# Performance work log

Hardware: AMD Instinct MI355X
Metric: run time of the kernel (lower is better)

The kernel has to match this reference:

```python
import jax, jax.numpy as jnp
import numpy as np

N = 100000   # nodes
E = 1600000  # edges (before self loops)
H = 4        # heads
C = 32       # per-head channels
D = H * C    # hidden_dim = 128
G = 64       # graphs in batch
L = 4        # num_layers
IN_DIM = 7
NEG_SLOPE = 0.2


def setup_inputs() -> dict:
    key = jax.random.key(0)
    ks = jax.random.split(key, 14)
    s = 0.1
    x = jax.random.normal(ks[0], (N, IN_DIM), jnp.float32)
    edge_index = jax.random.randint(ks[1], (2, E), 0, N, dtype=jnp.int32)
    batch = jnp.sort(jax.random.randint(ks[2], (N,), 0, G, dtype=jnp.int32))
    W0 = jax.random.normal(ks[3], (IN_DIM, D), jnp.float32) * s
    a_src0 = jax.random.normal(ks[4], (H, C), jnp.float32) * s
    a_dst0 = jax.random.normal(ks[5], (H, C), jnp.float32) * s
    b0 = jnp.zeros((D,), jnp.float32)
    Ws = jax.random.normal(ks[6], (L - 1, D, D), jnp.float32) * s
    a_srcs = jax.random.normal(ks[7], (L - 1, H, C), jnp.float32) * s
    a_dsts = jax.random.normal(ks[8], (L - 1, H, C), jnp.float32) * s
    bs = jnp.zeros((L - 1, D), jnp.float32)
    ln_g = jnp.ones((L, D), jnp.float32)
    ln_b = jnp.zeros((L, D), jnp.float32)
    return dict(x=x, edge_index=edge_index, batch=batch, W0=W0, a_src0=a_src0,
                a_dst0=a_dst0, b0=b0, Ws=Ws, a_srcs=a_srcs, a_dsts=a_dsts,
                bs=bs, ln_g=ln_g, ln_b=ln_b)


def _gat_layer(x, W, a_src, a_dst, b, src, dst):
    # x: [N, F_in] -> h: [N, H, C] (PyG GATConv: shared lin for src/dst)
    h = (x @ W).reshape(N, H, C)
    alpha_src = jnp.einsum('nhc,hc->nh', h, a_src)  # [N, H]
    alpha_dst = jnp.einsum('nhc,hc->nh', h, a_dst)  # [N, H]
    logits = jax.nn.leaky_relu(alpha_src[src] + alpha_dst[dst], NEG_SLOPE)  # [E', H]
    # segment softmax over edges grouped by destination node
    m = jax.ops.segment_max(logits, dst, num_segments=N)          # [N, H]
    e = jnp.exp(logits - m[dst])
    z = jax.ops.segment_sum(e, dst, num_segments=N)               # [N, H]
    alpha = e / (z[dst] + 1e-16)                                  # [E', H]
    msg = h[src] * alpha[..., None]                               # [E', H, C]
    out = jax.ops.segment_sum(msg, dst, num_segments=N)           # [N, H, C]
    return out.reshape(N, D) + b


def _layernorm(x, g, b):
    mu = jnp.mean(x, axis=-1, keepdims=True)
    var = jnp.var(x, axis=-1, keepdims=True)
    return (x - mu) * jax.lax.rsqrt(var + 1e-5) * g + b


def reference(x, edge_index, batch, W0, a_src0, a_dst0, b0, Ws, a_srcs, a_dsts, bs, ln_g, ln_b):
    # PyG GATConv default: add self loops
    loop = jnp.arange(N, dtype=edge_index.dtype)
    src = jnp.concatenate([edge_index[0], loop])
    dst = jnp.concatenate([edge_index[1], loop])
    h = x
    for i in range(L):
        if i == 0:
            W, asr, ads, b = W0, a_src0, a_dst0, b0
        else:
            W, asr, ads, b = Ws[i - 1], a_srcs[i - 1], a_dsts[i - 1], bs[i - 1]
        h_new = _gat_layer(h, W, asr, ads, b, src, dst)
        h_new = jax.nn.elu(_layernorm(h_new, ln_g[i], ln_b[i]))
        h = h + h_new if i > 0 else h_new  # dropout is identity in eval
    node_embeddings = h  # [N, D]
    sums = jax.ops.segment_sum(node_embeddings, batch, num_segments=G)  # [G, D]
    cnt = jax.ops.segment_sum(jnp.ones((N,), node_embeddings.dtype), batch, num_segments=G)
    graph_embedding = sums / jnp.maximum(cnt, 1.0)[:, None]
    return node_embeddings, graph_embedding
```

## Files before the change

kernel.cpp:

```cpp
#include <hip/hip_runtime.h>
#include <hip/hip_bf16.h>

#define NN 100000
#define NE 1600000
#define NH 4
#define NC 32
#define DD 128
#define NG 64
#define NIN 7

#define BSH 9
#define NBUK ((NN + 511) >> BSH)
#define SEGCAP 9600
#define CAPE (SEGCAP - 512)
#define CSRN (NBUK * SEGCAP)
#define NBBIN ((NE + 4095)/4096)

typedef __hip_bfloat16 bf16;
typedef __attribute__((ext_vector_type(8))) short short8;
typedef __attribute__((ext_vector_type(4))) float f32x4;
typedef __attribute__((ext_vector_type(2))) float f32x2;

__device__ __forceinline__ float b2f(const bf16 v){ return __bfloat162float(v); }

__device__ __forceinline__ float in_ld(const void* p, size_t i, int f32){
  return f32 ? ((const float*)p)[i] : b2f(((const bf16*)p)[i]);
}

__device__ __forceinline__ unsigned int bfbits(float v){
  bf16 b = __float2bfloat16(v);
  return (unsigned int)(*(unsigned short*)&b);
}

__global__ __launch_bounds__(256) void k_init(float* __restrict__ gsum, int* __restrict__ gcnt,
                                              int* __restrict__ bcur,
                                              const unsigned int* __restrict__ xb, int* __restrict__ flag){
  int i = blockIdx.x*256 + threadIdx.x;
  if (i < NG*DD) gsum[i] = 0.f;
  if (i < NG) gcnt[i] = 0;
  if (i < NBUK) bcur[i] = i * CAPE;
  if (blockIdx.x == 0 && threadIdx.x < 64){
    int t = threadIdx.x;
    int pl = 0;
    for (int j = t; j < 512; j += 64){
      float v = __uint_as_float(xb[j]);
      float a = fabsf(v);
      if (v == v && a < 1e6f && a > 1e-10f) pl++;
    }
    #pragma unroll
    for (int off = 32; off > 0; off >>= 1) pl += __shfl_down(pl, off);
    if (t == 0) *flag = (pl >= 384) ? 1 : 0;
  }
}

__global__ __launch_bounds__(256) void k_bin(const int* __restrict__ src, const int* __restrict__ dst,
                                             int* __restrict__ bcur, int2* __restrict__ gstag,
                                             const void* __restrict__ Ws, bf16* __restrict__ WT,
                                             const int* __restrict__ flag){
  if (blockIdx.x >= NBBIN){
    int l = blockIdx.x - NBBIN;
    int f32 = *flag;
    for (int idx = threadIdx.x; idx < DD*DD; idx += 256){
      int n = idx >> 7, k = idx & 127;
      WT[(size_t)l*DD*DD + idx] = __float2bfloat16(in_ld(Ws, (size_t)l*DD*DD + (size_t)k*DD + n, f32));
    }
    return;
  }
  __shared__ int cnt[NBUK], pref[NBUK+1], place[NBUK], gbase[NBUK];
  __shared__ int2 pairs[4096];
  int tid = threadIdx.x;
  for (int b = tid; b < NBUK; b += 256){ cnt[b]=0; place[b]=0; }
  __syncthreads();
  int e0 = blockIdx.x*4096;
  int s[16], d[16];
  #pragma unroll
  for (int i=0;i<16;i++){
    int e = e0 + i*256 + tid;
    s[i] = 0; d[i] = -1;
    if (e < NE){
      unsigned int us = (unsigned int)src[e]; if (us >= NN) us = 0;
      unsigned int ud = (unsigned int)dst[e]; if (ud >= NN) ud = 0;
      s[i] = (int)us; d[i] = (int)ud;
      atomicAdd(&cnt[ud>>BSH], 1);
    }
  }
  __syncthreads();
  if (tid == 0){
    int run = 0;
    for (int b=0;b<NBUK;b++){ pref[b] = run; run += cnt[b]; }
    pref[NBUK] = run;
  }
  __syncthreads();
  for (int b = tid; b < NBUK; b += 256){
    if (cnt[b] > 0) gbase[b] = atomicAdd(&bcur[b], cnt[b]);
  }
  __syncthreads();
  #pragma unroll
  for (int i=0;i<16;i++){
    if (d[i] >= 0){
      int b = d[i]>>BSH;
      int lp = atomicAdd(&place[b],1);
      pairs[pref[b]+lp] = make_int2(s[i], d[i]);
    }
  }
  __syncthreads();
  int tot = pref[NBUK];
  for (int j = tid; j < tot; j += 256){
    int2 pr = pairs[j];
    int b = pr.y>>BSH;
    int gidx = gbase[b] + (j - pref[b]);
    if (gidx >= b*CAPE && gidx < (b+1)*CAPE) gstag[gidx] = pr;
  }
}

__global__ __launch_bounds__(256) void k_bucket(const int2* __restrict__ gstag,
                                                const int* __restrict__ bcur,
                                                int* __restrict__ csr,
                                                int* __restrict__ offs, int* __restrict__ oend){
  __shared__ int seg[SEGCAP];
  __shared__ int lcnt[512];
  __shared__ int loff[512];
  __shared__ int pscan[256];
  int b = blockIdx.x, tid = threadIdx.x;
  int nstart = b << BSH;
  int nend = min(nstart + 512, NN);
  int nloc = nend - nstart;
  int base = b * SEGCAP;
  int stbase = b * CAPE;
  int ecnt = bcur[b] - stbase;
  ecnt = max(0, min(ecnt, CAPE));
  lcnt[tid]     = (tid < nloc) ? 1 : 0;
  lcnt[tid+256] = (tid+256 < nloc) ? 1 : 0;
  __syncthreads();
  for (int j = tid; j < ecnt; j += 256){
    int2 pr = gstag[stbase + j];
    int ln = pr.y - nstart;
    if (ln < 0 || ln >= nloc) ln = 0;
    atomicAdd(&lcnt[ln], 1);
  }
  __syncthreads();
  int c0 = lcnt[2*tid], c1 = lcnt[2*tid+1];
  int pairsum = c0 + c1;
  pscan[tid] = pairsum;
  __syncthreads();
  for (int off=1; off<256; off<<=1){
    int a = (tid >= off) ? pscan[tid-off] : 0;
    __syncthreads();
    pscan[tid] += a;
    __syncthreads();
  }
  int pexcl = pscan[tid] - pairsum;
  loff[2*tid]   = pexcl;
  loff[2*tid+1] = pexcl + c0;
  __syncthreads();
  int segN = pscan[255];
  if (segN > SEGCAP) segN = SEGCAP;
  if (tid < nloc){
    offs[nstart + tid] = base + loff[tid];
    oend[nstart + tid] = base + loff[tid] + lcnt[tid];
  }
  if (tid + 256 < nloc){
    offs[nstart + tid + 256] = base + loff[tid+256];
    oend[nstart + tid + 256] = base + loff[tid+256] + lcnt[tid+256];
  }
  __syncthreads();
  if (tid < nloc){ int p = loff[tid]; if (p < SEGCAP) seg[p] = nstart + tid; lcnt[tid] = 1; }
  if (tid + 256 < nloc){ int p = loff[tid+256]; if (p < SEGCAP) seg[p] = nstart + tid + 256; lcnt[tid+256] = 1; }
  __syncthreads();
  for (int j = tid; j < ecnt; j += 256){
    int2 pr = gstag[stbase + j];
    int ln = pr.y - nstart;
    if (ln < 0 || ln >= nloc) ln = 0;
    int p = atomicAdd(&lcnt[ln], 1);
    int idx = loff[ln] + p;
    if (idx >= 0 && idx < SEGCAP) seg[idx] = pr.x;
  }
  __syncthreads();
  for (int j = tid; j < segN; j += 256) csr[base + j] = seg[j];
}

__device__ __forceinline__ void alpha_red(float acc, float was, float wad, int d, int n,
                                          float* __restrict__ asrc, float* __restrict__ adst){
  float ps = acc*was, pd = acc*wad;
  #pragma unroll
  for (int off=16; off>0; off>>=1){
    ps += __shfl_down(ps, off, 32);
    pd += __shfl_down(pd, off, 32);
  }
  if ((d & 31) == 0){
    asrc[n*NH + (d>>5)] = ps;
    adst[n*NH + (d>>5)] = pd;
  }
}

__global__ __launch_bounds__(128) void k_gemm0(const void* __restrict__ x, const void* __restrict__ W,
    const void* __restrict__ aws, const void* __restrict__ awd,
    bf16* __restrict__ hproj,
    float* __restrict__ asrc, float* __restrict__ adst, const int* __restrict__ flag){
  int f32 = *flag;
  __shared__ float xr[4][NIN];
  int d = threadIdx.x;
  int n0 = blockIdx.x*4;
  if (d < 4*NIN) xr[d/NIN][d%NIN] = in_ld(x, (size_t)n0*NIN + d, f32);
  __syncthreads();
  float a0=0,a1=0,a2=0,a3=0;
  #pragma unroll
  for (int k=0;k<NIN;k++){
    float w = in_ld(W, (size_t)k*DD + d, f32);
    a0 += xr[0][k]*w; a1 += xr[1][k]*w; a2 += xr[2][k]*w; a3 += xr[3][k]*w;
  }
  hproj[(size_t)(n0+0)*DD+d]=__float2bfloat16(a0);
  hproj[(size_t)(n0+1)*DD+d]=__float2bfloat16(a1);
  hproj[(size_t)(n0+2)*DD+d]=__float2bfloat16(a2);
  hproj[(size_t)(n0+3)*DD+d]=__float2bfloat16(a3);
  float was = in_ld(aws, d, f32), wad = in_ld(awd, d, f32);
  alpha_red(a0, was, wad, d, n0+0, asrc, adst);
  alpha_red(a1, was, wad, d, n0+1, asrc, adst);
  alpha_red(a2, was, wad, d, n0+2, asrc, adst);
  alpha_red(a3, was, wad, d, n0+3, asrc, adst);
}

#define LDA 136
#define LDB 136

__global__ __launch_bounds__(256) void k_gemm_mfma(
    const bf16* __restrict__ resid,
    const bf16* __restrict__ WT, size_t wtoff,
    const void* __restrict__ aws, const void* __restrict__ awd, size_t aoff,
    bf16* __restrict__ hproj,
    float* __restrict__ asrc, float* __restrict__ adst,
    const int* __restrict__ flag)
{
  __shared__ bf16 sA[64*LDA];
  __shared__ bf16 sB[128*LDB];
  int f32 = *flag;
  int t = threadIdx.x;
  int n0 = blockIdx.x*64;

  {
    const uint4* srcv = (const uint4*)(WT + wtoff);
    #pragma unroll
    for (int i=0;i<8;i++){
      int u4 = t + 256*i;
      int row = u4 >> 4, c = u4 & 15;
      *(uint4*)(&sB[row*LDB + c*8]) = srcv[u4];
    }
  }
  {
    const uint4* av = (const uint4*)resid;
    #pragma unroll
    for (int i=0;i<4;i++){
      int u4 = t + 256*i;
      int row = u4 >> 4, c = u4 & 15;
      int gr = n0 + row;
      uint4 v = make_uint4(0,0,0,0);
      if (gr < NN) v = av[(size_t)gr*16 + c];
      *(uint4*)(&sA[row*LDA + c*8]) = v;
    }
  }
  __syncthreads();

  int wv = t >> 6, lane = t & 63;
  int m = lane & 15, kq = lane >> 4;
  int rowbase = wv*16;

  f32x4 acc[8];
  #pragma unroll
  for (int nt=0; nt<8; nt++) acc[nt] = (f32x4){0.f,0.f,0.f,0.f};

  #pragma unroll
  for (int ks=0; ks<4; ks++){
    short8 afrag = *(const short8*)(&sA[(rowbase + m)*LDA + ks*32 + kq*8]);
    #pragma unroll
    for (int nt=0; nt<8; nt++){
      short8 bfrag = *(const short8*)(&sB[(nt*16 + m)*LDB + ks*32 + kq*8]);
      acc[nt] = __builtin_amdgcn_mfma_f32_16x16x32_bf16(afrag, bfrag, acc[nt], 0, 0, 0);
    }
  }

  #pragma unroll
  for (int reg=0; reg<4; reg++){
    int gr = n0 + rowbase + kq*4 + reg;
    if (gr < NN){
      bf16* dst = hproj + (size_t)gr*DD + m;
      #pragma unroll
      for (int nt=0; nt<8; nt++)
        dst[nt*16] = __float2bfloat16(acc[nt][reg]);
    }
  }

  float avs[8], avd[8];
  #pragma unroll
  for (int nt=0; nt<8; nt++){
    avs[nt] = in_ld(aws, aoff + nt*16 + m, f32);
    avd[nt] = in_ld(awd, aoff + nt*16 + m, f32);
  }
  #pragma unroll
  for (int h=0; h<4; h++){
    #pragma unroll
    for (int reg=0; reg<4; reg++){
      float ps = acc[2*h][reg]*avs[2*h] + acc[2*h+1][reg]*avs[2*h+1];
      float pd = acc[2*h][reg]*avd[2*h] + acc[2*h+1][reg]*avd[2*h+1];
      #pragma unroll
      for (int off=1; off<16; off<<=1){
        ps += __shfl_xor(ps, off);
        pd += __shfl_xor(pd, off);
      }
      if (m == 0){
        int gr = n0 + rowbase + kq*4 + reg;
        if (gr < NN){
          asrc[gr*NH + h] = ps;
          adst[gr*NH + h] = pd;
        }
      }
    }
  }
}

__device__ __forceinline__ float4 edge_e(const float4 as, const float4 ad){
  float4 l, e;
  l.x = as.x + ad.x; l.y = as.y + ad.y; l.z = as.z + ad.z; l.w = as.w + ad.w;
  l.x = l.x > 0.f ? l.x : 0.2f*l.x;
  l.y = l.y > 0.f ? l.y : 0.2f*l.y;
  l.z = l.z > 0.f ? l.z : 0.2f*l.z;
  l.w = l.w > 0.f ? l.w : 0.2f*l.w;
  l.x = fminf(l.x, 30.f); l.y = fminf(l.y, 30.f);
  l.z = fminf(l.z, 30.f); l.w = fminf(l.w, 30.f);
  e.x = __expf(l.x); e.y = __expf(l.y); e.z = __expf(l.z); e.w = __expf(l.w);
  return e;
}

__device__ __forceinline__ float2 hp_ld2(const void* hp, int s, int lane){
  unsigned int hv = ((const unsigned int*)hp)[(size_t)s*64 + lane];
  return make_float2(__uint_as_float(hv << 16), __uint_as_float(hv & 0xFFFF0000u));
}

__device__ __forceinline__ void fma_row(const uint4 hv, const float al,
                                        f32x2& a0, f32x2& a1, f32x2& a2, f32x2& a3){
  f32x2 v0 = {__uint_as_float(hv.x << 16), __uint_as_float(hv.x & 0xFFFF0000u)};
  f32x2 v1 = {__uint_as_float(hv.y << 16), __uint_as_float(hv.y & 0xFFFF0000u)};
  f32x2 v2 = {__uint_as_float(hv.z << 16), __uint_as_float(hv.z & 0xFFFF0000u)};
  f32x2 v3 = {__uint_as_float(hv.w << 16), __uint_as_float(hv.w & 0xFFFF0000u)};
  a0 += v0 * al;
  a1 += v1 * al;
  a2 += v2 * al;
  a3 += v3 * al;
}

template<int U>
__global__ __launch_bounds__(256) void k_agg(const bf16* __restrict__ hproj,
    const float* __restrict__ asrc, const float* __restrict__ adst,
    const int* __restrict__ offs, const int* __restrict__ oend, const int* __restrict__ csr,
    bf16* __restrict__ resid,
    const void* __restrict__ bias, size_t boff,
    const void* __restrict__ lng, const void* __restrict__ lnb, size_t lnoff,
    const int* __restrict__ flag, const int first)
{
  __shared__ float s_al[4][256];
  __shared__ int   s_off[4][64];
  int f32 = *flag;
  int wid = threadIdx.x >> 6, lane = threadIdx.x & 63;
  int n = blockIdx.x*4 + wid;
  int beg = offs[n];
  int end = oend[n];
  beg = max(0, min(beg, CSRN));
  end = max(beg, min(end, CSRN));
  int deg = min(end - beg, 1024);
  const float4 ad = ((const float4*)adst)[n];
  int head = lane >> 4;
  const char* hpB = (const char*)hproj;
  float2 acc;

  if (deg <= 64){
    float4 e = make_float4(0,0,0,0);
    if (lane < deg){
      unsigned int us = (unsigned int)csr[beg+lane];
      if (us >= NN) us = 0;
      s_off[wid][lane] = (int)(us << 8);
      float4 as = ((const float4*)asrc)[us];
      e = edge_e(as, ad);
    }
    float4 zs = e;
    #pragma unroll
    for (int off=32; off>0; off>>=1){
      zs.x += __shfl_down(zs.x, off);
      zs.y += __shfl_down(zs.y, off);
      zs.z += __shfl_down(zs.z, off);
      zs.w += __shfl_down(zs.w, off);
    }
    float4 invz;
    invz.x = 1.f/(__shfl(zs.x,0)+1e-16f);
    invz.y = 1.f/(__shfl(zs.y,0)+1e-16f);
    invz.z = 1.f/(__shfl(zs.z,0)+1e-16f);
    invz.w = 1.f/(__shfl(zs.w,0)+1e-16f);
    if (lane < deg){
      s_al[wid][lane*4+0] = e.x*invz.x;
      s_al[wid][lane*4+1] = e.y*invz.y;
      s_al[wid][lane*4+2] = e.z*invz.z;
      s_al[wid][lane*4+3] = e.w*invz.w;
    }
    __threadfence_block();

    int qg = lane >> 4;
    int ql = lane & 15;
    int hq = ql >> 2;
    int qbyte = ql << 4;
    f32x2 a0 = {0.f,0.f}, a1 = {0.f,0.f}, a2 = {0.f,0.f}, a3 = {0.f,0.f};
    int t = 0;
    for (; t+U <= deg; t += U){
      uint4 h[U/4];
      #pragma unroll
      for (int u=0; u<U/4; u++){
        int j = t + 4*u + qg;
        unsigned int off = (unsigned int)s_off[wid][j] + qbyte;
        h[u] = *(const uint4*)(hpB + off);
      }
      #pragma unroll
      for (int u=0; u<U/4; u++){
        int j = t + 4*u + qg;
        float al = s_al[wid][j*4 + hq];
        fma_row(h[u], al, a0, a1, a2, a3);
      }
    }
    for (; t+4 <= deg; t += 4){
      int j = t + qg;
      unsigned int off = (unsigned int)s_off[wid][j] + qbyte;
      const uint4 hv = *(const uint4*)(hpB + off);
      float al = s_al[wid][j*4 + hq];
      fma_row(hv, al, a0, a1, a2, a3);
    }
    if (t < deg){
      int j = t + qg;
      if (j < deg){
        unsigned int off = (unsigned int)s_off[wid][j] + qbyte;
        const uint4 hv = *(const uint4*)(hpB + off);
        float al = s_al[wid][j*4 + hq];
        fma_row(hv, al, a0, a1, a2, a3);
      }
    }

    #pragma unroll
    for (int off = 16; off < 64; off <<= 1){
      a0.x += __shfl_xor(a0.x, off); a0.y += __shfl_xor(a0.y, off);
      a1.x += __shfl_xor(a1.x, off); a1.y += __shfl_xor(a1.y, off);
      a2.x += __shfl_xor(a2.x, off); a2.y += __shfl_xor(a2.y, off);
      a3.x += __shfl_xor(a3.x, off); a3.y += __shfl_xor(a3.y, off);
    }
    __threadfence_block();
    if (qg == 0){
      float* red = &s_al[wid][0];
      red[ql*8+0] = a0.x; red[ql*8+1] = a0.y;
      red[ql*8+2] = a1.x; red[ql*8+3] = a1.y;
      red[ql*8+4] = a2.x; red[ql*8+5] = a2.y;
      red[ql*8+6] = a3.x; red[ql*8+7] = a3.y;
    }
    __threadfence_block();
    acc = make_float2(s_al[wid][2*lane], s_al[wid][2*lane+1]);
  } else {
    f32x2 ac0 = {0.f,0.f};
    float4 zs = make_float4(0,0,0,0);
    for (int j=lane; j<deg; j+=64){
      unsigned int us = (unsigned int)csr[beg+j];
      if (us >= NN) us = 0;
      float4 as = ((const float4*)asrc)[us];
      float4 e = edge_e(as, ad);
      zs.x+=e.x; zs.y+=e.y; zs.z+=e.z; zs.w+=e.w;
    }
    #pragma unroll
    for (int off=32; off>0; off>>=1){
      zs.x += __shfl_down(zs.x, off);
      zs.y += __shfl_down(zs.y, off);
      zs.z += __shfl_down(zs.z, off);
      zs.w += __shfl_down(zs.w, off);
    }
    float4 invz;
    invz.x = 1.f/(__shfl(zs.x,0)+1e-16f);
    invz.y = 1.f/(__shfl(zs.y,0)+1e-16f);
    invz.z = 1.f/(__shfl(zs.z,0)+1e-16f);
    invz.w = 1.f/(__shfl(zs.w,0)+1e-16f);
    int nch = (deg+63)>>6;
    for (int c2=0;c2<nch;c2++){
      int base = c2<<6, j = base+lane;
      int sreg = 0;
      __threadfence_block();
      if (j < deg){
        unsigned int us = (unsigned int)csr[beg+j];
        if (us >= NN) us = 0;
        sreg = (int)us;
        float4 as = ((const float4*)asrc)[us];
        float4 e = edge_e(as, ad);
        s_al[wid][lane*4+0]=e.x*invz.x;
        s_al[wid][lane*4+1]=e.y*invz.y;
        s_al[wid][lane*4+2]=e.z*invz.z;
        s_al[wid][lane*4+3]=e.w*invz.w;
      }
      __threadfence_block();
      int cnt = min(64, deg-base);
      int head2 = lane >> 4;
      for (int t2=0;t2<cnt;t2++){
        int s = __shfl(sreg, t2);
        float a = s_al[wid][t2*4+head2];
        float2 hv = hp_ld2(hproj, s, lane);
        ac0.x += hv.x*a;
        ac0.y += hv.y*a;
      }
    }
    acc = make_float2(ac0.x, ac0.y);
  }

  float vx = acc.x + in_ld(bias, boff + 2*lane,   f32);
  float vy = acc.y + in_ld(bias, boff + 2*lane+1, f32);
  float s1 = vx+vy, s2 = vx*vx+vy*vy;
  #pragma unroll
  for (int off=32; off>0; off>>=1){
    s1 += __shfl_down(s1, off);
    s2 += __shfl_down(s2, off);
  }
  float mean = __shfl(s1,0) * (1.f/DD);
  float msq  = __shfl(s2,0) * (1.f/DD);
  float var  = fmaxf(msq - mean*mean, 0.f);
  float r = rsqrtf(var + 1e-5f);
  float yx = (vx-mean)*r*in_ld(lng, lnoff+2*lane,   f32) + in_ld(lnb, lnoff+2*lane,   f32);
  float yy = (vy-mean)*r*in_ld(lng, lnoff+2*lane+1, f32) + in_ld(lnb, lnoff+2*lane+1, f32);
  yx = yx>0.f ? yx : expm1f(yx);
  yy = yy>0.f ? yy : expm1f(yy);
  float2 res;
  if (first){
    res = make_float2(yx, yy);
  } else {
    unsigned int pu = ((const unsigned int*)resid)[(size_t)n*64 + lane];
    res = make_float2(__uint_as_float(pu << 16) + yx,
                      __uint_as_float(pu & 0xFFFF0000u) + yy);
  }
  unsigned int pk = bfbits(res.x) | (bfbits(res.y) << 16);
  ((unsigned int*)resid)[(size_t)n*64 + lane] = pk;
}

__global__ __launch_bounds__(128) void k_pool(const bf16* __restrict__ resid, void* __restrict__ dout,
    const int* __restrict__ batch, float* __restrict__ gsum, int* __restrict__ gcnt,
    const int* __restrict__ flag){
  __shared__ int sb[64];
  int f32 = *flag;
  int d = threadIdx.x;
  int n0 = blockIdx.x*64;
  int cnt = min(64, NN - n0);
  if (d < cnt){
    unsigned int b = (unsigned int)batch[n0 + d];
    if (b >= NG) b = 0;
    sb[d] = (int)b;
  }
  __syncthreads();
  float local = 0.f;
  int cur = sb[0];
  for (int i=0;i<cnt;i++){
    int b = sb[i];
    if (b != cur){
      atomicAdd(&gsum[cur*DD + d], local);
      local = 0.f; cur = b;
    }
    size_t idx = (size_t)(n0+i)*DD + d;
    float v = b2f(resid[idx]);
    if (f32) ((float*)dout)[idx] = v;
    else     ((bf16*)dout)[idx] = resid[idx];
    local += v;
  }
  atomicAdd(&gsum[cur*DD + d], local);
  if (d == 0){
    int lc = 0; int c2 = sb[0];
    for (int i=0;i<cnt;i++){
      int b = sb[i];
      if (b != c2){ atomicAdd(&gcnt[c2], lc); lc = 0; c2 = b; }
      lc++;
    }
    atomicAdd(&gcnt[c2], lc);
  }
}

__global__ __launch_bounds__(128) void k_final(const float* __restrict__ gsum, const int* __restrict__ gcnt,
                                               void* __restrict__ dout, const int* __restrict__ flag){
  int f32 = *flag;
  int i = blockIdx.x*128 + threadIdx.x;
  if (i < NG*DD){
    float c = (float)gcnt[i>>7];
    if (c < 1.f) c = 1.f;
    float val = gsum[i] / c;
    if (f32) ((float*)dout)[(size_t)NN*DD + i] = val;
    else     ((bf16*)dout)[(size_t)NN*DD + i] = __float2bfloat16(val);
  }
}

extern "C" void kernel_launch(void* const* d_in, const int* in_sizes, int n_in,
                              void* d_out, int out_size, void* d_ws, size_t ws_size,
                              hipStream_t stream){
  const void* x      = d_in[0];
  const int*  ei     = (const int*) d_in[1];
  const int*  batch  = (const int*) d_in[2];
  const void* W0     = d_in[3];
  const void* asrc0  = d_in[4];
  const void* adst0  = d_in[5];
  const void* b0     = d_in[6];
  const void* Ws     = d_in[7];
  const void* asrcs  = d_in[8];
  const void* adsts  = d_in[9];
  const void* bs     = d_in[10];
  const void* lng    = d_in[11];
  const void* lnb    = d_in[12];

  const int* srcs = ei;
  const int* dsts = ei + NE;

  uintptr_t p0 = (uintptr_t)d_ws;
  uintptr_t p = p0;
  auto alloc = [&](size_t bytes)->void* {
    void* r = (void*)p; p += (bytes + 255) & ~(size_t)255; return r;
  };
  int*   csr    = (int*)  alloc((size_t)CSRN*4);
  int*   offs   = (int*)  alloc((size_t)NN*4);
  int*   oend   = (int*)  alloc((size_t)NN*4);
  float* asrc   = (float*)alloc((size_t)NN*NH*4);
  float* adst   = (float*)alloc((size_t)NN*NH*4);
  float* gsum   = (float*)alloc((size_t)NG*DD*4);
  int*   gcnt   = (int*)  alloc(NG*4);
  int*   flag   = (int*)  alloc(256);
  int*   bcur   = (int*)  alloc((size_t)NBUK*4);
  int2*  gstag  = (int2*) alloc((size_t)NBUK*CAPE*8);
  bf16*  wt     = (bf16*) alloc((size_t)3*DD*DD*2);
  bf16*  hproj  = (bf16*) alloc((size_t)NN*DD*2);
  bf16*  resid  = (bf16*) alloc((size_t)NN*DD*2);

  const int NB = (NN + 255)/256;

  k_init<<<NB, 256, 0, stream>>>(gsum, gcnt, bcur, (const unsigned int*)x, flag);
  k_bin<<<NBBIN + 3, 256, 0, stream>>>(srcs, dsts, bcur, gstag, Ws, wt, flag);
  k_bucket<<<NBUK, 256, 0, stream>>>(gstag, bcur, csr, offs, oend);

  const int GEMM_B = (NN + 63)/64;

  k_gemm0<<<NN/4, 128, 0, stream>>>(x, W0, asrc0, adst0, hproj, asrc, adst, flag);
  k_agg<4><<<NN/4, 256, 0, stream>>>(hproj, asrc, adst, offs, oend, csr, resid,
                                     b0, 0, lng, lnb, 0, flag, 1);
  k_gemm_mfma<<<GEMM_B, 256, 0, stream>>>(resid, wt, 0, asrcs, adsts, 0,
                                          hproj, asrc, adst, flag);
  k_agg<8><<<NN/4, 256, 0, stream>>>(hproj, asrc, adst, offs, oend, csr, resid,
                                     bs, 0, lng, lnb, (size_t)1*DD, flag, 0);
  k_gemm_mfma<<<GEMM_B, 256, 0, stream>>>(resid, wt, (size_t)1*DD*DD, asrcs, adsts, (size_t)1*DD,
                                          hproj, asrc, adst, flag);
  k_agg<16><<<NN/4, 256, 0, stream>>>(hproj, asrc, adst, offs, oend, csr, resid,
                                      bs, (size_t)1*DD, lng, lnb, (size_t)2*DD, flag, 0);
  k_gemm_mfma<<<GEMM_B, 256, 0, stream>>>(resid, wt, (size_t)2*DD*DD, asrcs, adsts, (size_t)2*DD,
                                          hproj, asrc, adst, flag);
  k_agg<8><<<NN/4, 256, 0, stream>>>(hproj, asrc, adst, offs, oend, csr, resid,
                                     bs, (size_t)2*DD, lng, lnb, (size_t)3*DD, flag, 0);

  k_pool<<<(NN+63)/64, 128, 0, stream>>>(resid, d_out, batch, gsum, gcnt, flag);
  k_final<<<(NG*DD+127)/128, 128, 0, stream>>>(gsum, gcnt, d_out, flag);
}
```

Baseline: 625.7 us.

## Vectorize pooling with block-local group reduction and unify aggregation template parameter

Rewrites the pooling kernel to use 256 threads, each loading a 16-byte vector of eight bf16 values per row. Per-block sums for the first and last graph are reduced in shared memory before a single global atomic per column, replacing per-thread serial scans. The aggregation launches now all use the same template parameter instead of a mix of values, and the layer loop is folded. The inner-loop head index in the aggregation is switched from a local to an existing variable, which depends on that variable matching the old one.

```diff
diff --git a/kernel.cpp b/kernel.cpp
--- a/kernel.cpp
+++ b/kernel.cpp
@@ -496,10 +496,9 @@
       }
       __threadfence_block();
       int cnt = min(64, deg-base);
-      int head2 = lane >> 4;
       for (int t2=0;t2<cnt;t2++){
         int s = __shfl(sreg, t2);
-        float a = s_al[wid][t2*4+head2];
+        float a = s_al[wid][t2*4+head];
         float2 hv = hp_ld2(hproj, s, lane);
         ac0.x += hv.x*a;
         ac0.y += hv.y*a;
@@ -536,43 +535,87 @@
   ((unsigned int*)resid)[(size_t)n*64 + lane] = pk;
 }
 
-__global__ __launch_bounds__(128) void k_pool(const bf16* __restrict__ resid, void* __restrict__ dout,
+__global__ __launch_bounds__(256) void k_pool(const bf16* __restrict__ resid, void* __restrict__ dout,
     const int* __restrict__ batch, float* __restrict__ gsum, int* __restrict__ gcnt,
     const int* __restrict__ flag){
   __shared__ int sb[64];
+  __shared__ float s_sum[2][DD];
+  __shared__ int s_cnt[2];
   int f32 = *flag;
-  int d = threadIdx.x;
+  int t = threadIdx.x;
+  int s = t >> 4, ql = t & 15;
   int n0 = blockIdx.x*64;
   int cnt = min(64, NN - n0);
-  if (d < cnt){
-    unsigned int b = (unsigned int)batch[n0 + d];
-    if (b >= NG) b = 0;
-    sb[d] = (int)b;
-  }
-  __syncthreads();
-  float local = 0.f;
-  int cur = sb[0];
-  for (int i=0;i<cnt;i++){
-    int b = sb[i];
-    if (b != cur){
-      atomicAdd(&gsum[cur*DD + d], local);
-      local = 0.f; cur = b;
-    }
-    size_t idx = (size_t)(n0+i)*DD + d;
-    float v = b2f(resid[idx]);
-    if (f32) ((float*)dout)[idx] = v;
-    else     ((bf16*)dout)[idx] = resid[idx];
-    local += v;
-  }
-  atomicAdd(&gsum[cur*DD + d], local);
-  if (d == 0){
-    int lc = 0; int c2 = sb[0];
-    for (int i=0;i<cnt;i++){
-      int b = sb[i];
-      if (b != c2){ atomicAdd(&gcnt[c2], lc); lc = 0; c2 = b; }
-      lc++;
-    }
-    atomicAdd(&gcnt[c2], lc);
+  if (t < 64){
+    int bi = 0;
+    if (t < cnt){
+      unsigned int b = (unsigned int)batch[n0 + t];
+      if (b >= NG) b = 0;
+      bi = (int)b;
+    }
+    sb[t] = bi;
+  }
+  ((float*)s_sum)[t] = 0.f;
+  if (t < 2) s_cnt[t] = 0;
+  __syncthreads();
+  int g0 = sb[0];
+  int g1 = sb[cnt-1];
+  if (t < cnt){
+    int b = sb[t];
+    if (b == g0) atomicAdd(&s_cnt[0], 1);
+    else if (b == g1) atomicAdd(&s_cnt[1], 1);
+    else atomicAdd(&gcnt[b], 1);
+  }
+  float acc0[8] = {0,0,0,0,0,0,0,0};
+  float acc1[8] = {0,0,0,0,0,0,0,0};
+  const uint4* rv = (const uint4*)resid;
+  #pragma unroll
+  for (int k=0;k<4;k++){
+    int r = k*16 + s;
+    if (r < cnt){
+      int n = n0 + r;
+      uint4 hv = rv[(size_t)n*16 + ql];
+      float v[8];
+      v[0]=__uint_as_float(hv.x<<16); v[1]=__uint_as_float(hv.x&0xFFFF0000u);
+      v[2]=__uint_as_float(hv.y<<16); v[3]=__uint_as_float(hv.y&0xFFFF0000u);
+      v[4]=__uint_as_float(hv.z<<16); v[5]=__uint_as_float(hv.z&0xFFFF0000u);
+      v[6]=__uint_as_float(hv.w<<16); v[7]=__uint_as_float(hv.w&0xFFFF0000u);
+      if (f32){
+        float4* dp = (float4*)((char*)dout + (size_t)n*512 + ql*32);
+        dp[0] = make_float4(v[0],v[1],v[2],v[3]);
+        dp[1] = make_float4(v[4],v[5],v[6],v[7]);
+      } else {
+        *(uint4*)((char*)dout + (size_t)n*256 + ql*16) = hv;
+      }
+      int b = sb[r];
+      if (b == g0){
+        #pragma unroll
+        for (int i=0;i<8;i++) acc0[i] += v[i];
+      } else if (b == g1){
+        #pragma unroll
+        for (int i=0;i<8;i++) acc1[i] += v[i];
+      } else {
+        #pragma unroll
+        for (int i=0;i<8;i++) atomicAdd(&gsum[b*DD + ql*8 + i], v[i]);
+      }
+    }
+  }
+  int c0 = ql*8;
+  int twog = (g1 != g0);
+  #pragma unroll
+  for (int i=0;i<8;i++){
+    atomicAdd(&s_sum[0][c0+i], acc0[i]);
+    if (twog) atomicAdd(&s_sum[1][c0+i], acc1[i]);
+  }
+  __syncthreads();
+  if (t < DD){
+    atomicAdd(&gsum[g0*DD + t], s_sum[0][t]);
+  } else if (twog && t < 2*DD){
+    atomicAdd(&gsum[g1*DD + (t-DD)], s_sum[1][t-DD]);
+  }
+  if (t == 0){
+    atomicAdd(&gcnt[g0], s_cnt[0]);
+    if (twog) atomicAdd(&gcnt[g1], s_cnt[1]);
   }
 }
 
@@ -637,21 +680,18 @@
   const int GEMM_B = (NN + 63)/64;
 
   k_gemm0<<<NN/4, 128, 0, stream>>>(x, W0, asrc0, adst0, hproj, asrc, adst, flag);
-  k_agg<4><<<NN/4, 256, 0, stream>>>(hproj, asrc, adst, offs, oend, csr, resid,
+  k_agg<8><<<NN/4, 256, 0, stream>>>(hproj, asrc, adst, offs, oend, csr, resid,
                                      b0, 0, lng, lnb, 0, flag, 1);
-  k_gemm_mfma<<<GEMM_B, 256, 0, stream>>>(resid, wt, 0, asrcs, adsts, 0,
-                                          hproj, asrc, adst, flag);
-  k_agg<8><<<NN/4, 256, 0, stream>>>(hproj, asrc, adst, offs, oend, csr, resid,
-                                     bs, 0, lng, lnb, (size_t)1*DD, flag, 0);
-  k_gemm_mfma<<<GEMM_B, 256, 0, stream>>>(resid, wt, (size_t)1*DD*DD, asrcs, adsts, (size_t)1*DD,
-                                          hproj, asrc, adst, flag);
-  k_agg<16><<<NN/4, 256, 0, stream>>>(hproj, asrc, adst, offs, oend, csr, resid,
-                                      bs, (size_t)1*DD, lng, lnb, (size_t)2*DD, flag, 0);
-  k_gemm_mfma<<<GEMM_B, 256, 0, stream>>>(resid, wt, (size_t)2*DD*DD, asrcs, adsts, (size_t)2*DD,
-                                          hproj, asrc, adst, flag);
-  k_agg<8><<<NN/4, 256, 0, stream>>>(hproj, asrc, adst, offs, oend, csr, resid,
-                                     bs, (size_t)2*DD, lng, lnb, (size_t)3*DD, flag, 0);
-
-  k_pool<<<(NN+63)/64, 128, 0, stream>>>(resid, d_out, batch, gsum, gcnt, flag);
+  for (int l=1; l<4; l++){
+    size_t wtoff = (size_t)(l-1)*DD*DD;
+    size_t aoff  = (size_t)(l-1)*DD;
+    k_gemm_mfma<<<GEMM_B, 256, 0, stream>>>(resid, wt, wtoff,
+                                            asrcs, adsts, aoff,
+                                            hproj, asrc, adst, flag);
+    k_agg<8><<<NN/4, 256, 0, stream>>>(hproj, asrc, adst, offs, oend, csr, resid,
+                                       bs, (size_t)(l-1)*DD, lng, lnb, (size_t)l*DD, flag, 0);
+  }
+
+  k_pool<<<(NN+63)/64, 256, 0, stream>>>(resid, d_out, batch, gsum, gcnt, flag);
   k_final<<<(NG*DD+127)/128, 128, 0, stream>>>(gsum, gcnt, d_out, flag);
 }
```

New measurement: 615.1 us. About the same (-1.7%).
